# Optimization experiments

Hardware: AMD Instinct MI355X
Metric: run time of the kernel (lower is better)

## Reference

```python
import jax, jax.numpy as jnp
import numpy as np

N_NODES = 100_000
N_EDGES = 1_600_000
B = 2
CH_N = 8; CH_E = 8; CH_K = 8; HID = 16
DT = 1.0
MAX_VALUE = 1e6


def _mlp(x, w1, b1, w2, b2):
    return jnp.tanh(x @ w1 + b1) @ w2 + b2


def _soft_clamp(x):
    return MAX_VALUE * jnp.tanh(x / MAX_VALUE)


def _seg_attn(logit, msg, seg, n):
    # logit [E], msg [E,C]; softmax over edges sharing a segment, weighted sum.
    mx = jax.ops.segment_max(logit, seg, num_segments=n)
    ex = jnp.exp(logit - mx[seg])
    den = jax.ops.segment_sum(ex, seg, num_segments=n)
    num = jax.ops.segment_sum(ex[:, None] * msg, seg, num_segments=n)
    return num / (den[:, None] + 1e-10)


def setup_inputs() -> dict:
    key = jax.random.key(0)
    ks = jax.random.split(key, 20)
    r = lambda k, shp, sc=0.3: (jax.random.normal(k, shp, dtype=jnp.float32) * sc)
    inp = {
        "nodes": jax.random.normal(ks[0], (B, N_NODES, CH_N), dtype=jnp.float32),
        "edges": jax.random.normal(ks[1], (B, N_EDGES, CH_E), dtype=jnp.float32),
        "msg_w1": r(ks[2], (2 * CH_N + CH_E, HID)),
        "msg_b1": jnp.zeros((HID,), jnp.float32),
        "msg_w2": r(ks[3], (HID, 2 * CH_N + CH_E)),
        "msg_b2": jnp.zeros((2 * CH_N + CH_E,), jnp.float32),
        "att_w1": r(ks[4], (CH_N, HID)),
        "att_b1": jnp.zeros((HID,), jnp.float32),
        "att_w2": r(ks[5], (HID, 4 * CH_K)),
        "att_b2": jnp.zeros((4 * CH_K,), jnp.float32),
        "upd_w1": r(ks[6], (3 * CH_N, HID)),
        "upd_b1": jnp.zeros((HID,), jnp.float32),
        "upd_w2": r(ks[7], (HID, CH_N)),
        "upd_b2": jnp.zeros((CH_N,), jnp.float32),
        "sources": jax.random.randint(ks[8], (N_EDGES,), 0, N_NODES, dtype=jnp.int32).astype(jnp.int64) if False else jax.random.randint(ks[8], (N_EDGES,), 0, N_NODES),
        "targets": jax.random.randint(ks[9], (N_EDGES,), 0, N_NODES),
    }
    return inp


def reference(nodes, edges, msg_w1, msg_b1, msg_w2, msg_b2,
              att_w1, att_b1, att_w2, att_b2,
              upd_w1, upd_b1, upd_w2, upd_b2,
              sources, targets):
    # --- per-edge messages: gather endpoint nodes, concat with edge state ---
    m_x = jnp.concatenate([nodes[:, sources], nodes[:, targets], edges], axis=2)  # [B,E,2*ch_n+ch_e]
    m = _mlp(m_x, msg_w1, msg_b1, msg_w2, msg_b2)
    m_a = m[..., :CH_N]                 # message to source node
    m_b = m[..., CH_N:2 * CH_N]         # message to target node
    m_ab = m[..., 2 * CH_N:]            # edge update

    # --- attention keys/queries per node (4*ch_k) ---
    att = _mlp(nodes, att_w1, att_b1, att_w2, att_b2)  # [B,N,4*ch_k]
    a_key, a_query, b_key, b_query = jnp.split(att, 4, axis=2)
    scale = 1.0 / np.sqrt(CH_K).astype(np.float32)
    logit_a = (a_query[:, sources] * b_key[:, targets]).sum(-1) * scale  # [B,E]
    logit_b = (b_query[:, targets] * a_key[:, sources]).sum(-1) * scale

    agg_a = jax.vmap(lambda l, ms: _seg_attn(l, ms, sources, N_NODES))(logit_a, m_a)  # [B,N,ch_n]
    agg_b = jax.vmap(lambda l, ms: _seg_attn(l, ms, targets, N_NODES))(logit_b, m_b)

    # --- node update ---
    u_x = jnp.concatenate([nodes, agg_a, agg_b], axis=2)  # [B,N,3*ch_n]
    upd = _mlp(u_x, upd_w1, upd_b1, upd_w2, upd_b2)

    new_nodes = _soft_clamp(nodes + DT * upd)
    new_edges = _soft_clamp(edges + DT * m_ab)
    return new_nodes, new_edges
```

## Files before the change

kernel.cpp:

```cpp
#include <hip/hip_runtime.h>

#define NN 100000
#define NE 1600000
#define NB 2
#define CH 8
#define HID 16
#define NTILES 98

typedef unsigned int uint;
typedef float f32x4 __attribute__((ext_vector_type(4)));

__device__ __forceinline__ float soft_clamp(float x) {
    float y = x * 1e-6f;
    return x * (1.0f - 0.33333333f * y * y);
}
__device__ __forceinline__ float fast_tanh(float x) {
    float ax = fabsf(x);
    float t = __expf(-2.0f * ax);
    float r = (1.0f - t) / (1.0f + t);
    return copysignf(r, x);
}
__device__ __forceinline__ void load8(const float* __restrict__ p, float* x) {
    float4 a = ((const float4*)p)[0];
    float4 b = ((const float4*)p)[1];
    x[0]=a.x; x[1]=a.y; x[2]=a.z; x[3]=a.w; x[4]=b.x; x[5]=b.y; x[6]=b.z; x[7]=b.w;
}
__device__ __forceinline__ void store8(float* __restrict__ p, const float* x) {
    ((float4*)p)[0] = make_float4(x[0],x[1],x[2],x[3]);
    ((float4*)p)[1] = make_float4(x[4],x[5],x[6],x[7]);
}
__device__ __forceinline__ void f4w(float* p, float4 v){ p[0]=v.x; p[1]=v.y; p[2]=v.z; p[3]=v.w; }

__device__ __forceinline__ uint bfu(float x) {
    uint u = __float_as_uint(x);
    return (u + 0x7fffu + ((u >> 16) & 1u)) >> 16;
}
__device__ __forceinline__ float ubf(uint u) { return __uint_as_float(u << 16); }

__device__ __forceinline__ ushort f2h(float x) {
    _Float16 h = (_Float16)x;
    union { _Float16 h; ushort u; } c; c.h = h; return c.u;
}
__device__ __forceinline__ float h2f(uint u) {
    union { ushort u; _Float16 h; } c; c.u = (ushort)u; return (float)c.h;
}
__device__ __forceinline__ float dot8h(uint4 a, uint4 b) {
    const uint* pa = &a.x; const uint* pb = &b.x;
    float s = 0.0f;
#pragma unroll
    for (int i = 0; i < 4; i++) {
        s += h2f(pa[i] & 0xffffu) * h2f(pb[i] & 0xffffu);
        s += h2f(pa[i] >> 16)     * h2f(pb[i] >> 16);
    }
    return s;
}

__device__ __forceinline__ void acc8(float* h, uint4 v, const float* __restrict__ w) {
    const uint* p = &v.x;
#pragma unroll
    for (int i = 0; i < 4; i++) {
        float x0 = h2f(p[i] & 0xffffu), x1 = h2f(p[i] >> 16);
#pragma unroll
        for (int j = 0; j < HID; j++) h[j] += x0 * w[(2*i)*HID + j];
#pragma unroll
        for (int j = 0; j < HID; j++) h[j] += x1 * w[(2*i+1)*HID + j];
    }
}

__global__ void __launch_bounds__(256)
att_pack_kernel(const float* __restrict__ nodes,
                const float* __restrict__ w1, const float* __restrict__ b1,
                const float* __restrict__ w2, const float* __restrict__ b2,
                uint4* __restrict__ S, uint4* __restrict__ T,
                float4* __restrict__ nodesP) {
    __shared__ float sw1[CH*HID], sb1[HID], sw2[HID*32], sb2[32];
    int tid = threadIdx.x;
    for (int i = tid; i < CH*HID; i += 256) sw1[i] = w1[i];
    for (int i = tid; i < HID; i += 256) sb1[i] = b1[i];
    for (int i = tid; i < HID*32; i += 256) sw2[i] = w2[i];
    for (int i = tid; i < 32; i += 256) sb2[i] = b2[i];
    __syncthreads();
    int n = blockIdx.x * 256 + tid;
    if (n >= NN) return;
    int b = blockIdx.y;
    size_t base = (size_t)b * NN + n;

    float x[CH];
    load8(nodes + base * CH, x);
    nodesP[(size_t)n*4 + b*2]     = make_float4(x[0],x[1],x[2],x[3]);
    nodesP[(size_t)n*4 + b*2 + 1] = make_float4(x[4],x[5],x[6],x[7]);

    float h[HID];
#pragma unroll
    for (int j = 0; j < HID; j++) {
        float acc = sb1[j];
#pragma unroll
        for (int i = 0; i < CH; i++) acc += x[i] * sw1[i*HID + j];
        h[j] = fast_tanh(acc);
    }
    float o[32];
#pragma unroll
    for (int k = 0; k < 32; k++) {
        float acc = sb2[k];
#pragma unroll
        for (int j = 0; j < HID; j++) acc += h[j] * sw2[j*32 + k];
        o[k] = acc;
    }
    uint4 nx, ak, aq, bk, bq;
    nx.x=f2h(x[0]) |(f2h(x[1]) <<16); nx.y=f2h(x[2]) |(f2h(x[3]) <<16);
    nx.z=f2h(x[4]) |(f2h(x[5]) <<16); nx.w=f2h(x[6]) |(f2h(x[7]) <<16);
    ak.x=f2h(o[0]) |(f2h(o[1]) <<16); ak.y=f2h(o[2]) |(f2h(o[3]) <<16);
    ak.z=f2h(o[4]) |(f2h(o[5]) <<16); ak.w=f2h(o[6]) |(f2h(o[7]) <<16);
    aq.x=f2h(o[8]) |(f2h(o[9]) <<16); aq.y=f2h(o[10])|(f2h(o[11])<<16);
    aq.z=f2h(o[12])|(f2h(o[13])<<16); aq.w=f2h(o[14])|(f2h(o[15])<<16);
    bk.x=f2h(o[16])|(f2h(o[17])<<16); bk.y=f2h(o[18])|(f2h(o[19])<<16);
    bk.z=f2h(o[20])|(f2h(o[21])<<16); bk.w=f2h(o[22])|(f2h(o[23])<<16);
    bq.x=f2h(o[24])|(f2h(o[25])<<16); bq.y=f2h(o[26])|(f2h(o[27])<<16);
    bq.z=f2h(o[28])|(f2h(o[29])<<16); bq.w=f2h(o[30])|(f2h(o[31])<<16);
    size_t sl = (size_t)n*8 + b*4;
    S[sl+0] = nx; S[sl+1] = ak; S[sl+2] = aq;
    T[sl+0] = nx; T[sl+1] = bk; T[sl+2] = bq;
}

__global__ void __launch_bounds__(256)
hist_rank_kernel(const int* __restrict__ src, const int* __restrict__ tgt,
                 int* __restrict__ cntA, int* __restrict__ cntB,
                 int* __restrict__ rankA, int* __restrict__ rankB) {
    int e = blockIdx.x * 256 + threadIdx.x;
    if (e >= NE) return;
    rankA[e] = atomicAdd(&cntA[src[e]], 1);
    rankB[e] = atomicAdd(&cntB[tgt[e]], 1);
}

__global__ void __launch_bounds__(256)
scan_part_kernel(const int* __restrict__ cnt, int* __restrict__ part) {
    int y = blockIdx.y;
    const int* c = cnt + (size_t)y * NN;
    __shared__ int s[256];
    int t = threadIdx.x, bx = blockIdx.x;
    int base = bx * 1024 + t * 4;
    int sum = 0;
#pragma unroll
    for (int k = 0; k < 4; k++) { int i = base + k; sum += (i < NN) ? c[i] : 0; }
    s[t] = sum; __syncthreads();
    for (int off = 128; off > 0; off >>= 1) { if (t < off) s[t] += s[t + off]; __syncthreads(); }
    if (t == 0) part[y * 256 + bx] = s[0];
}

__global__ void __launch_bounds__(256)
scan_top_kernel(int* __restrict__ part, int* __restrict__ rowA, int* __restrict__ rowB) {
    int y = blockIdx.y; int t = threadIdx.x;
    __shared__ int s[256];
    int v = (t < NTILES) ? part[y * 256 + t] : 0;
    s[t] = v; __syncthreads();
    for (int off = 1; off < 256; off <<= 1) {
        int x = (t >= off) ? s[t - off] : 0;
        __syncthreads();
        s[t] += x;
        __syncthreads();
    }
    part[y * 256 + t] = t ? s[t - 1] : 0;
    if (t == 0) (y ? rowB : rowA)[NN] = NE;
}

__global__ void __launch_bounds__(256)
scan_down_kernel(const int* __restrict__ cnt, const int* __restrict__ part,
                 int* __restrict__ rowA, int* __restrict__ rowB) {
    int y = blockIdx.y;
    const int* c = cnt + (size_t)y * NN;
    int* row = y ? rowB : rowA;
    __shared__ int s[256];
    int t = threadIdx.x, bx = blockIdx.x;
    int base = bx * 1024 + t * 4;
    int v[4]; int tsum = 0;
#pragma unroll
    for (int k = 0; k < 4; k++) { int i = base + k; v[k] = (i < NN) ? c[i] : 0; tsum += v[k]; }
    s[t] = tsum; __syncthreads();
    for (int off = 1; off < 256; off <<= 1) {
        int x = (t >= off) ? s[t - off] : 0;
        __syncthreads();
        s[t] += x;
        __syncthreads();
    }
    int run = part[y * 256 + bx] + s[t] - tsum;
#pragma unroll
    for (int k = 0; k < 4; k++) {
        int i = base + k;
        if (i < NN) row[i] = run;
        run += v[k];
    }
}

__global__ void __launch_bounds__(256)
fill_kernel(const int* __restrict__ src, const int* __restrict__ tgt,
            const int* __restrict__ rowA, const int* __restrict__ rowB,
            const int* __restrict__ rankA, const int* __restrict__ rankB,
            int* __restrict__ eidA, int* __restrict__ eidB) {
    int e = blockIdx.x * 256 + threadIdx.x;
    if (e >= NE) return;
    eidA[rowA[src[e]] + rankA[e]] = e;
    eidB[rowB[tgt[e]] + rankB[e]] = e;
}

__global__ void __launch_bounds__(256, 2)
edge_kernel(const uint4* __restrict__ S, const uint4* __restrict__ T,
            const float* __restrict__ edges,
            const int* __restrict__ src, const int* __restrict__ tgt,
            const float* __restrict__ w1, const float* __restrict__ b1,
            const float* __restrict__ w2, const float* __restrict__ b2,
            float* __restrict__ out_edges,
            uint4* __restrict__ recA, uint4* __restrict__ recB) {
    __shared__ float sw1[24*HID], sb1[HID], sw2[HID*24], sb2[24];
    int tid = threadIdx.x;
    for (int i = tid; i < 24*HID; i += 256) sw1[i] = w1[i];
    for (int i = tid; i < HID; i += 256) sb1[i] = b1[i];
    for (int i = tid; i < HID*24; i += 256) sw2[i] = w2[i];
    for (int i = tid; i < 24; i += 256) sb2[i] = b2[i];
    __syncthreads();
    int b = blockIdx.x;
    int e = blockIdx.y * 256 + tid;
    int s = src[e], t = tgt[e];
    const float scale = 0.35355339059327373f;

    size_t sl = (size_t)s*8 + b*4, tl = (size_t)t*8 + b*4;
    uint4 sn = S[sl], ak = S[sl+1], aq = S[sl+2];
    uint4 tn = T[tl], bk = T[tl+1], bq = T[tl+2];
    f32x4 e0, e1;
    {
        const f32x4* ep = (const f32x4*)(edges + ((size_t)b*NE + e)*CH);
        e0 = __builtin_nontemporal_load(ep);
        e1 = __builtin_nontemporal_load(ep + 1);
    }

    float la = scale * dot8h(aq, bk);
    float lb = scale * dot8h(bq, ak);

    float h[HID];
#pragma unroll
    for (int j = 0; j < HID; j++) h[j] = sb1[j];
    acc8(h, sn, sw1);
    acc8(h, tn, sw1 + 8*HID);
    float ef[8];
    ef[0]=e0.x; ef[1]=e0.y; ef[2]=e0.z; ef[3]=e0.w;
    ef[4]=e1.x; ef[5]=e1.y; ef[6]=e1.z; ef[7]=e1.w;
#pragma unroll
    for (int i = 0; i < 8; i++) {
#pragma unroll
        for (int j = 0; j < HID; j++) h[j] += ef[i] * sw1[(16+i)*HID + j];
    }
#pragma unroll
    for (int j = 0; j < HID; j++) h[j] = fast_tanh(h[j]);

    float m[24];
#pragma unroll
    for (int k = 0; k < 24; k++) {
        float acc = sb2[k];
#pragma unroll
        for (int j = 0; j < HID; j++) acc += h[j] * sw2[j*24 + k];
        m[k] = acc;
    }

    {
        f32x4* op = (f32x4*)(out_edges + ((size_t)b*NE + e)*CH);
        f32x4 o0, o1;
        o0.x = soft_clamp(ef[0] + m[16]); o0.y = soft_clamp(ef[1] + m[17]);
        o0.z = soft_clamp(ef[2] + m[18]); o0.w = soft_clamp(ef[3] + m[19]);
        o1.x = soft_clamp(ef[4] + m[20]); o1.y = soft_clamp(ef[5] + m[21]);
        o1.z = soft_clamp(ef[6] + m[22]); o1.w = soft_clamp(ef[7] + m[23]);
        __builtin_nontemporal_store(o0, op);
        __builtin_nontemporal_store(o1, op + 1);
    }

    recA[(size_t)e*4 + b*2] = make_uint4(__float_as_uint(la),
                                         bfu(m[0]) | (bfu(m[1]) << 16),
                                         bfu(m[2]) | (bfu(m[3]) << 16),
                                         bfu(m[4]) | (bfu(m[5]) << 16));
    recA[(size_t)e*4 + b*2 + 1] = make_uint4(bfu(m[6]) | (bfu(m[7]) << 16), 0u, 0u, 0u);
    recB[(size_t)e*4 + b*2] = make_uint4(__float_as_uint(lb),
                                         bfu(m[8])  | (bfu(m[9])  << 16),
                                         bfu(m[10]) | (bfu(m[11]) << 16),
                                         bfu(m[12]) | (bfu(m[13]) << 16));
    recB[(size_t)e*4 + b*2 + 1] = make_uint4(bfu(m[14]) | (bfu(m[15]) << 16), 0u, 0u, 0u);
}

__device__ __forceinline__ void aggregate(int beg, int end, const int* __restrict__ eid,
                                          const uint4* __restrict__ rec,
                                          float* __restrict__ o0, float* __restrict__ o1) {
    float mx0 = -1e30f, den0 = 0.0f, num0[CH];
    float mx1 = -1e30f, den1 = 0.0f, num1[CH];
#pragma unroll
    for (int c = 0; c < CH; c++) { num0[c] = 0.0f; num1[c] = 0.0f; }
    for (int i = beg; i < end; ++i) {
        int e = eid[i];
        const uint4* P = rec + (size_t)e*4;
        uint4 q0 = P[0], q1 = P[1], q2 = P[2], q3 = P[3];
        {
            float l = __uint_as_float(q0.x);
            float nm = fmaxf(mx0, l);
            float r = __expf(mx0 - nm), w = __expf(l - nm);
            mx0 = nm; den0 = den0 * r + w;
            float mm[CH];
            mm[0]=ubf(q0.y&0xffffu); mm[1]=ubf(q0.y>>16);
            mm[2]=ubf(q0.z&0xffffu); mm[3]=ubf(q0.z>>16);
            mm[4]=ubf(q0.w&0xffffu); mm[5]=ubf(q0.w>>16);
            mm[6]=ubf(q1.x&0xffffu); mm[7]=ubf(q1.x>>16);
#pragma unroll
            for (int c = 0; c < CH; c++) num0[c] = num0[c] * r + w * mm[c];
        }
        {
            float l = __uint_as_float(q2.x);
            float nm = fmaxf(mx1, l);
            float r = __expf(mx1 - nm), w = __expf(l - nm);
            mx1 = nm; den1 = den1 * r + w;
            float mm[CH];
            mm[0]=ubf(q2.y&0xffffu); mm[1]=ubf(q2.y>>16);
            mm[2]=ubf(q2.z&0xffffu); mm[3]=ubf(q2.z>>16);
            mm[4]=ubf(q2.w&0xffffu); mm[5]=ubf(q2.w>>16);
            mm[6]=ubf(q3.x&0xffffu); mm[7]=ubf(q3.x>>16);
#pragma unroll
            for (int c = 0; c < CH; c++) num1[c] = num1[c] * r + w * mm[c];
        }
    }
    float i0 = 1.0f / (den0 + 1e-10f), i1 = 1.0f / (den1 + 1e-10f);
#pragma unroll
    for (int c = 0; c < CH; c++) { o0[c] = num0[c] * i0; o1[c] = num1[c] * i1; }
}

__device__ __forceinline__ void upd_mlp(const float* __restrict__ in,
                                        const float* __restrict__ sw1, const float* __restrict__ sb1,
                                        const float* __restrict__ sw2, const float* __restrict__ sb2,
                                        float* __restrict__ no) {
    float h[HID];
#pragma unroll
    for (int j = 0; j < HID; j++) {
        float acc = sb1[j];
#pragma unroll
        for (int i = 0; i < 24; i++) acc += in[i] * sw1[i*HID + j];
        h[j] = fast_tanh(acc);
    }
#pragma unroll
    for (int k = 0; k < CH; k++) {
        float acc = sb2[k];
#pragma unroll
        for (int j = 0; j < HID; j++) acc += h[j] * sw2[j*CH + k];
        no[k] = soft_clamp(in[k] + acc);
    }
}

__global__ void __launch_bounds__(256, 2)
node_kernel(const float4* __restrict__ nodesP,
            const int* __restrict__ rowA, const int* __restrict__ rowB,
            const int* __restrict__ eidA, const int* __restrict__ eidB,
            const uint4* __restrict__ recA, const uint4* __restrict__ recB,
            const float* __restrict__ w1, const float* __restrict__ b1,
            const float* __restrict__ w2, const float* __restrict__ b2,
            float* __restrict__ out_nodes) {
    __shared__ float sw1[24*HID], sb1[HID], sw2[HID*CH], sb2[CH];
    int tid = threadIdx.x;
    for (int i = tid; i < 24*HID; i += 256) sw1[i] = w1[i];
    for (int i = tid; i < HID; i += 256) sb1[i] = b1[i];
    for (int i = tid; i < HID*CH; i += 256) sw2[i] = w2[i];
    for (int i = tid; i < CH; i += 256) sb2[i] = b2[i];
    __syncthreads();
    int n = blockIdx.x * 256 + tid;
    if (n >= NN) return;

    float in0[24], in1[24];
    float4 np0 = nodesP[(size_t)n*4+0], np1 = nodesP[(size_t)n*4+1];
    float4 np2 = nodesP[(size_t)n*4+2], np3 = nodesP[(size_t)n*4+3];
    f4w(in0, np0); f4w(in0+4, np1);
    f4w(in1, np2); f4w(in1+4, np3);

    aggregate(rowA[n], rowA[n+1], eidA, recA, in0 + 8,  in1 + 8);
    aggregate(rowB[n], rowB[n+1], eidB, recB, in0 + 16, in1 + 16);

    float no0[CH], no1[CH];
    upd_mlp(in0, sw1, sb1, sw2, sb2, no0);
    upd_mlp(in1, sw1, sb1, sw2, sb2, no1);
    store8(out_nodes + (size_t)n*CH, no0);
    store8(out_nodes + (size_t)NN*CH + (size_t)n*CH, no1);
}

extern "C" void kernel_launch(void* const* d_in, const int* in_sizes, int n_in,
                              void* d_out, int out_size, void* d_ws, size_t ws_size,
                              hipStream_t stream) {
    const float* nodes  = (const float*)d_in[0];
    const float* edges  = (const float*)d_in[1];
    const float* msg_w1 = (const float*)d_in[2];
    const float* msg_b1 = (const float*)d_in[3];
    const float* msg_w2 = (const float*)d_in[4];
    const float* msg_b2 = (const float*)d_in[5];
    const float* att_w1 = (const float*)d_in[6];
    const float* att_b1 = (const float*)d_in[7];
    const float* att_w2 = (const float*)d_in[8];
    const float* att_b2 = (const float*)d_in[9];
    const float* upd_w1 = (const float*)d_in[10];
    const float* upd_b1 = (const float*)d_in[11];
    const float* upd_w2 = (const float*)d_in[12];
    const float* upd_b2 = (const float*)d_in[13];
    const int*   sources = (const int*)d_in[14];
    const int*   targets = (const int*)d_in[15];

    float* out       = (float*)d_out;
    float* out_nodes = out;
    float* out_edges = out + (size_t)NB * NN * CH;

    char* wp = (char*)d_ws;
    size_t off = 0;
    auto take = [&](size_t bytes) -> char* {
        char* p = wp + off;
        off = (off + bytes + 255) & ~(size_t)255;
        return p;
    };
    uint4*  S      = (uint4*)take((size_t)NN * NB * 64);
    uint4*  T      = (uint4*)take((size_t)NN * NB * 64);
    float4* nodesP = (float4*)take((size_t)NN * 64);
    int*    cnt    = (int*)take((size_t)2 * NN * 4);
    int*    rowA   = (int*)take((size_t)(NN + 1) * 4);
    int*    rowB   = (int*)take((size_t)(NN + 1) * 4);
    int*    part   = (int*)take((size_t)2 * 256 * 4);
    int*    rankA  = (int*)take((size_t)NE * 4);
    int*    rankB  = (int*)take((size_t)NE * 4);
    int*    eidA   = (int*)take((size_t)NE * 4);
    int*    eidB   = (int*)take((size_t)NE * 4);
    uint4*  recA   = (uint4*)take((size_t)NE * 64);
    uint4*  recB   = (uint4*)take((size_t)NE * 64);
    int* cntA = cnt, *cntB = cnt + NN;

    dim3 gn((NN + 255) / 256, NB);
    dim3 gn1((NN + 255) / 256);
    dim3 ge1((NE + 255) / 256);
    dim3 geb(NB, NE / 256);
    dim3 gs(NTILES, 2);
    dim3 gt(1, 2);

    (void)hipMemsetAsync(cnt, 0, (size_t)2 * NN * 4, stream);
    att_pack_kernel<<<gn, 256, 0, stream>>>(nodes, att_w1, att_b1, att_w2, att_b2,
                                            S, T, nodesP);
    hist_rank_kernel<<<ge1, 256, 0, stream>>>(sources, targets, cntA, cntB, rankA, rankB);
    scan_part_kernel<<<gs, 256, 0, stream>>>(cnt, part);
    scan_top_kernel<<<gt, 256, 0, stream>>>(part, rowA, rowB);
    scan_down_kernel<<<gs, 256, 0, stream>>>(cnt, part, rowA, rowB);
    fill_kernel<<<ge1, 256, 0, stream>>>(sources, targets, rowA, rowB, rankA, rankB,
                                         eidA, eidB);
    edge_kernel<<<geb, 256, 0, stream>>>(S, T, edges, sources, targets,
                                         msg_w1, msg_b1, msg_w2, msg_b2,
                                         out_edges, recA, recB);
    node_kernel<<<gn1, 256, 0, stream>>>(nodesP, rowA, rowB, eidA, eidB, recA, recB,
                                         upd_w1, upd_b1, upd_w2, upd_b2, out_nodes);
}
```

Before: 597.0 us.

## Fuse CSR fill into edge kernel and split node kernel per batch

The separate fill kernel that scatters edge ids into the CSR arrays is removed. Its work now runs inside the edge kernel for batch index 0, which saves a launch and re-reading src/tgt. The node kernel now uses one thread per (node, batch) pair instead of one thread handling both batches, which doubles the thread count and halves per-thread registers, and its launch bound drops the min-blocks hint. Each thread now reads only its half of the edge records, but the eid and row lookups are duplicated across the two batch threads.

```diff
diff --git a/kernel.cpp b/kernel.cpp
--- a/kernel.cpp
+++ b/kernel.cpp
@@ -191,21 +191,13 @@
     }
 }
 
-__global__ void __launch_bounds__(256)
-fill_kernel(const int* __restrict__ src, const int* __restrict__ tgt,
-            const int* __restrict__ rowA, const int* __restrict__ rowB,
-            const int* __restrict__ rankA, const int* __restrict__ rankB,
-            int* __restrict__ eidA, int* __restrict__ eidB) {
-    int e = blockIdx.x * 256 + threadIdx.x;
-    if (e >= NE) return;
-    eidA[rowA[src[e]] + rankA[e]] = e;
-    eidB[rowB[tgt[e]] + rankB[e]] = e;
-}
-
 __global__ void __launch_bounds__(256, 2)
 edge_kernel(const uint4* __restrict__ S, const uint4* __restrict__ T,
             const float* __restrict__ edges,
             const int* __restrict__ src, const int* __restrict__ tgt,
+            const int* __restrict__ rowA, const int* __restrict__ rowB,
+            const int* __restrict__ rankA, const int* __restrict__ rankB,
+            int* __restrict__ eidA, int* __restrict__ eidB,
             const float* __restrict__ w1, const float* __restrict__ b1,
             const float* __restrict__ w2, const float* __restrict__ b2,
             float* __restrict__ out_edges,
@@ -222,6 +214,11 @@
     int s = src[e], t = tgt[e];
     const float scale = 0.35355339059327373f;
 
+    if (b == 0) {
+        eidA[rowA[s] + rankA[e]] = e;
+        eidB[rowB[t] + rankB[e]] = e;
+    }
+
     size_t sl = (size_t)s*8 + b*4, tl = (size_t)t*8 + b*4;
     uint4 sn = S[sl], ak = S[sl+1], aq = S[sl+2];
     uint4 tn = T[tl], bk = T[tl+1], bq = T[tl+2];
@@ -283,71 +280,34 @@
     recB[(size_t)e*4 + b*2 + 1] = make_uint4(bfu(m[14]) | (bfu(m[15]) << 16), 0u, 0u, 0u);
 }
 
-__device__ __forceinline__ void aggregate(int beg, int end, const int* __restrict__ eid,
-                                          const uint4* __restrict__ rec,
-                                          float* __restrict__ o0, float* __restrict__ o1) {
-    float mx0 = -1e30f, den0 = 0.0f, num0[CH];
-    float mx1 = -1e30f, den1 = 0.0f, num1[CH];
-#pragma unroll
-    for (int c = 0; c < CH; c++) { num0[c] = 0.0f; num1[c] = 0.0f; }
+__device__ __forceinline__ void aggregate1(int beg, int end, const int* __restrict__ eid,
+                                           const uint4* __restrict__ rec, int boff,
+                                           float* __restrict__ o) {
+    float mx = -1e30f, den = 0.0f, num[CH];
+#pragma unroll
+    for (int c = 0; c < CH; c++) num[c] = 0.0f;
     for (int i = beg; i < end; ++i) {
         int e = eid[i];
-        const uint4* P = rec + (size_t)e*4;
-        uint4 q0 = P[0], q1 = P[1], q2 = P[2], q3 = P[3];
-        {
-            float l = __uint_as_float(q0.x);
-            float nm = fmaxf(mx0, l);
-            float r = __expf(mx0 - nm), w = __expf(l - nm);
-            mx0 = nm; den0 = den0 * r + w;
-            float mm[CH];
-            mm[0]=ubf(q0.y&0xffffu); mm[1]=ubf(q0.y>>16);
-            mm[2]=ubf(q0.z&0xffffu); mm[3]=ubf(q0.z>>16);
-            mm[4]=ubf(q0.w&0xffffu); mm[5]=ubf(q0.w>>16);
-            mm[6]=ubf(q1.x&0xffffu); mm[7]=ubf(q1.x>>16);
-#pragma unroll
-            for (int c = 0; c < CH; c++) num0[c] = num0[c] * r + w * mm[c];
-        }
-        {
-            float l = __uint_as_float(q2.x);
-            float nm = fmaxf(mx1, l);
-            float r = __expf(mx1 - nm), w = __expf(l - nm);
-            mx1 = nm; den1 = den1 * r + w;
-            float mm[CH];
-            mm[0]=ubf(q2.y&0xffffu); mm[1]=ubf(q2.y>>16);
-            mm[2]=ubf(q2.z&0xffffu); mm[3]=ubf(q2.z>>16);
-            mm[4]=ubf(q2.w&0xffffu); mm[5]=ubf(q2.w>>16);
-            mm[6]=ubf(q3.x&0xffffu); mm[7]=ubf(q3.x>>16);
-#pragma unroll
-            for (int c = 0; c < CH; c++) num1[c] = num1[c] * r + w * mm[c];
-        }
-    }
-    float i0 = 1.0f / (den0 + 1e-10f), i1 = 1.0f / (den1 + 1e-10f);
-#pragma unroll
-    for (int c = 0; c < CH; c++) { o0[c] = num0[c] * i0; o1[c] = num1[c] * i1; }
-}
-
-__device__ __forceinline__ void upd_mlp(const float* __restrict__ in,
-                                        const float* __restrict__ sw1, const float* __restrict__ sb1,
-                                        const float* __restrict__ sw2, const float* __restrict__ sb2,
-                                        float* __restrict__ no) {
-    float h[HID];
-#pragma unroll
-    for (int j = 0; j < HID; j++) {
-        float acc = sb1[j];
-#pragma unroll
-        for (int i = 0; i < 24; i++) acc += in[i] * sw1[i*HID + j];
-        h[j] = fast_tanh(acc);
-    }
-#pragma unroll
-    for (int k = 0; k < CH; k++) {
-        float acc = sb2[k];
-#pragma unroll
-        for (int j = 0; j < HID; j++) acc += h[j] * sw2[j*CH + k];
-        no[k] = soft_clamp(in[k] + acc);
-    }
-}
-
-__global__ void __launch_bounds__(256, 2)
+        const uint4* P = rec + (size_t)e*4 + boff;
+        uint4 q0 = P[0], q1 = P[1];
+        float l = __uint_as_float(q0.x);
+        float nm = fmaxf(mx, l);
+        float r = __expf(mx - nm), w = __expf(l - nm);
+        mx = nm; den = den * r + w;
+        float mm[CH];
+        mm[0]=ubf(q0.y&0xffffu); mm[1]=ubf(q0.y>>16);
+        mm[2]=ubf(q0.z&0xffffu); mm[3]=ubf(q0.z>>16);
+        mm[4]=ubf(q0.w&0xffffu); mm[5]=ubf(q0.w>>16);
+        mm[6]=ubf(q1.x&0xffffu); mm[7]=ubf(q1.x>>16);
+#pragma unroll
+        for (int c = 0; c < CH; c++) num[c] = num[c] * r + w * mm[c];
+    }
+    float inv = 1.0f / (den + 1e-10f);
+#pragma unroll
+    for (int c = 0; c < CH; c++) o[c] = num[c] * inv;
+}
+
+__global__ void __launch_bounds__(256)
 node_kernel(const float4* __restrict__ nodesP,
             const int* __restrict__ rowA, const int* __restrict__ rowB,
             const int* __restrict__ eidA, const int* __restrict__ eidB,
@@ -362,23 +322,34 @@
     for (int i = tid; i < HID*CH; i += 256) sw2[i] = w2[i];
     for (int i = tid; i < CH; i += 256) sb2[i] = b2[i];
     __syncthreads();
-    int n = blockIdx.x * 256 + tid;
+    int g = blockIdx.x * 256 + tid;
+    int n = g >> 1, b = g & 1;
     if (n >= NN) return;
 
-    float in0[24], in1[24];
-    float4 np0 = nodesP[(size_t)n*4+0], np1 = nodesP[(size_t)n*4+1];
-    float4 np2 = nodesP[(size_t)n*4+2], np3 = nodesP[(size_t)n*4+3];
-    f4w(in0, np0); f4w(in0+4, np1);
-    f4w(in1, np2); f4w(in1+4, np3);
-
-    aggregate(rowA[n], rowA[n+1], eidA, recA, in0 + 8,  in1 + 8);
-    aggregate(rowB[n], rowB[n+1], eidB, recB, in0 + 16, in1 + 16);
-
-    float no0[CH], no1[CH];
-    upd_mlp(in0, sw1, sb1, sw2, sb2, no0);
-    upd_mlp(in1, sw1, sb1, sw2, sb2, no1);
-    store8(out_nodes + (size_t)n*CH, no0);
-    store8(out_nodes + (size_t)NN*CH + (size_t)n*CH, no1);
+    float in[24];
+    float4 np0 = nodesP[(size_t)n*4 + b*2], np1 = nodesP[(size_t)n*4 + b*2 + 1];
+    f4w(in, np0); f4w(in + 4, np1);
+
+    aggregate1(rowA[n], rowA[n+1], eidA, recA, b*2, in + 8);
+    aggregate1(rowB[n], rowB[n+1], eidB, recB, b*2, in + 16);
+
+    float h[HID];
+#pragma unroll
+    for (int j = 0; j < HID; j++) {
+        float acc = sb1[j];
+#pragma unroll
+        for (int i = 0; i < 24; i++) acc += in[i] * sw1[i*HID + j];
+        h[j] = fast_tanh(acc);
+    }
+    float no[CH];
+#pragma unroll
+    for (int k = 0; k < CH; k++) {
+        float acc = sb2[k];
+#pragma unroll
+        for (int j = 0; j < HID; j++) acc += h[j] * sw2[j*CH + k];
+        no[k] = soft_clamp(in[k] + acc);
+    }
+    store8(out_nodes + ((size_t)b*NN + n)*CH, no);
 }
 
 extern "C" void kernel_launch(void* const* d_in, const int* in_sizes, int n_in,
@@ -428,7 +399,7 @@
     int* cntA = cnt, *cntB = cnt + NN;
 
     dim3 gn((NN + 255) / 256, NB);
-    dim3 gn1((NN + 255) / 256);
+    dim3 gn2((2*NN + 255) / 256);
     dim3 ge1((NE + 255) / 256);
     dim3 geb(NB, NE / 256);
     dim3 gs(NTILES, 2);
@@ -441,11 +412,10 @@
     scan_part_kernel<<<gs, 256, 0, stream>>>(cnt, part);
     scan_top_kernel<<<gt, 256, 0, stream>>>(part, rowA, rowB);
     scan_down_kernel<<<gs, 256, 0, stream>>>(cnt, part, rowA, rowB);
-    fill_kernel<<<ge1, 256, 0, stream>>>(sources, targets, rowA, rowB, rankA, rankB,
-                                         eidA, eidB);
     edge_kernel<<<geb, 256, 0, stream>>>(S, T, edges, sources, targets,
+                                         rowA, rowB, rankA, rankB, eidA, eidB,
                                          msg_w1, msg_b1, msg_w2, msg_b2,
                                          out_edges, recA, recB);
-    node_kernel<<<gn1, 256, 0, stream>>>(nodesP, rowA, rowB, eidA, eidB, recA, recB,
+    node_kernel<<<gn2, 256, 0, stream>>>(nodesP, rowA, rowB, eidA, eidB, recA, recB,
                                          upd_w1, upd_b1, upd_w2, upd_b2, out_nodes);
 }
```

Result: slower. 610.0 us (+2.2%).
